# Optimization experiments

Hardware: AMD Instinct MI355X
Metric: run time of the kernel (lower is better)

The kernel has to match this reference:

```python
import jax, jax.numpy as jnp
import numpy as np

FLOW_NUM = 16


def _mlp(z0, p):
    # z0: [B,1]; p = (W1,b1,W2,b2,W3,b3,W4,b4)
    W1, b1, W2, b2, W3, b3, W4, b4 = p
    h = jax.nn.relu(z0 @ W1 + b1)      # [B,10]
    h = jax.nn.relu(h @ W2 + b2)       # [B,10]
    h = jnp.tanh(h @ W3 + b3)          # [B,20]
    return h @ W4 + b4                 # [B,2]


def _forward(inputs, W1, b1, W2, b2, W3, b3, W4, b4):
    x = inputs.astype(jnp.float32)
    z0 = x[:, 0:1]
    z1 = x[:, 1:2]

    def step(carry, p):
        z0_old, z1_old, logdet = carry
        out = _mlp(z0_old, p)                    # [B,2]
        log_scale = out[:, 0:1]                  # log of affine scale
        shift = out[:, 1:2]
        z1_new = jnp.exp(log_scale) * z1_old + shift
        # swap roles for next flow (as in the torch code)
        return (z1_new, z0_old, logdet + log_scale), None

    (z0f, z1f, logdet), _ = jax.lax.scan(
        step, (z0, z1, jnp.zeros_like(z0)), (W1, b1, W2, b2, W3, b3, W4, b4))
    # after the loop: z0_new = z0_old (carry[1]), z1_new = carry[0]
    z0_new, z1_new = z1f, z0f
    # log of standard-normal density product (same math as log(pz))
    log_pz = -0.5 * (z0_new ** 2 + z1_new ** 2) - jnp.log(2.0 * jnp.pi)
    return log_pz + logdet, jnp.concatenate((z0_new, z1_new), axis=1)


def setup_inputs() -> dict:
    key = jax.random.key(0)
    ks = jax.random.split(key, 9)
    B, F = 2097152, FLOW_NUM

    def glorot(k, shape):
        fan_in, fan_out = shape[-2], shape[-1]
        lim = np.sqrt(6.0 / (fan_in + fan_out))
        return jax.random.uniform(k, shape, jnp.float32, -lim, lim)

    return {
        "inputs": jax.random.normal(ks[0], (B, 2), jnp.float32),
        "W1": glorot(ks[1], (F, 1, 10)),  "b1": jnp.zeros((F, 10), jnp.float32),
        "W2": glorot(ks[2], (F, 10, 10)), "b2": jnp.zeros((F, 10), jnp.float32),
        "W3": glorot(ks[3], (F, 10, 20)), "b3": jnp.zeros((F, 20), jnp.float32),
        "W4": glorot(ks[4], (F, 20, 2)),  "b4": jnp.zeros((F, 2), jnp.float32),
    }


def reference(inputs, W1, b1, W2, b2, W3, b3, W4, b4):
    return _forward(inputs, W1, b1, W2, b2, W3, b3, W4, b4)
```

## Files before the change

### kernel.cpp

```cpp
#include <hip/hip_runtime.h>
#include <hip/hip_fp16.h>

#define FLOWS 16
#define NE 2048
#define TAB_DWORDS (FLOWS * NE)
#define TAB_BYTES  (TAB_DWORDS * 4)

__device__ __forceinline__ float2 eval_mlp(int l, float z0,
        const float* __restrict__ W1, const float* __restrict__ B1,
        const float* __restrict__ W2, const float* __restrict__ B2,
        const float* __restrict__ W3, const float* __restrict__ B3,
        const float* __restrict__ W4, const float* __restrict__ B4) {
    const float* w1 = W1 + l * 10;
    const float* c1 = B1 + l * 10;
    const float* w2 = W2 + l * 100;
    const float* c2 = B2 + l * 10;
    const float* w3 = W3 + l * 200;
    const float* c3 = B3 + l * 20;
    const float* w4 = W4 + l * 40;
    const float* c4 = B4 + l * 2;

    float h1[10];
#pragma unroll
    for (int j = 0; j < 10; ++j)
        h1[j] = fmaxf(fmaf(z0, w1[j], c1[j]), 0.0f);

    float h2[10];
#pragma unroll
    for (int j = 0; j < 10; ++j) {
        float acc = c2[j];
#pragma unroll
        for (int i = 0; i < 10; ++i) acc = fmaf(h1[i], w2[i * 10 + j], acc);
        h2[j] = fmaxf(acc, 0.0f);
    }

    float h3[20];
#pragma unroll
    for (int j = 0; j < 20; ++j) {
        float acc = c3[j];
#pragma unroll
        for (int i = 0; i < 10; ++i) acc = fmaf(h2[i], w3[i * 20 + j], acc);
        h3[j] = tanhf(acc);
    }

    float ls = c4[0], sh = c4[1];
#pragma unroll
    for (int i = 0; i < 20; ++i) {
        ls = fmaf(h3[i], w4[i * 2 + 0], ls);
        sh = fmaf(h3[i], w4[i * 2 + 1], sh);
    }
    return make_float2(ls * 1.4426950408889634f, sh);
}

__device__ __forceinline__ float node_z0(int i) {
    float u = fmaf((float)i, 30.0f / 2048.0f, -15.0f);
    float m = 0.125f * (exp2f(fabsf(u)) - 1.0f);
    return u < 0.0f ? -m : m;
}

__global__ __launch_bounds__(256) void build_table_f16(
        const float* __restrict__ W1, const float* __restrict__ B1,
        const float* __restrict__ W2, const float* __restrict__ B2,
        const float* __restrict__ W3, const float* __restrict__ B3,
        const float* __restrict__ W4, const float* __restrict__ B4,
        unsigned int* __restrict__ gtab) {
    int t = blockIdx.x * blockDim.x + threadIdx.x;
    if (t >= TAB_DWORDS) return;
    int l = t >> 11, i = t & (NE - 1);
    float2 r = eval_mlp(l, node_z0(i), W1, B1, W2, B2, W3, B3, W4, B4);
    unsigned int lo = (unsigned int)__half_as_ushort(__float2half_rn(r.x));
    unsigned int hi = (unsigned int)__half_as_ushort(__float2half_rn(r.y));
    gtab[t] = lo | (hi << 16);
}

#define TROWS 8

__global__ __launch_bounds__(1024) void realnvp_lds(
        const float* __restrict__ x,
        const unsigned int* __restrict__ gtab,
        float* __restrict__ out, int nrows) {
    __shared__ unsigned int st[TAB_DWORDS];

    {
        uint4* d = (uint4*)st;
        const uint4* s = (const uint4*)gtab;
        for (int k = threadIdx.x; k < TAB_DWORDS / 4; k += 1024) d[k] = s[k];
    }
    __syncthreads();

    const int rbase = blockIdx.x * (TROWS * 1024) + threadIdx.x;

    float z0[TROWS], z1[TROWS], ld2[TROWS];
#pragma unroll
    for (int r = 0; r < TROWS; ++r) {
        const int row = rbase + r * 1024;
        float2 xv = (row < nrows) ? reinterpret_cast<const float2*>(x)[row]
                                  : make_float2(0.0f, 0.0f);
        z0[r] = xv.x; z1[r] = xv.y; ld2[r] = 0.0f;
    }

    const float INV_DU = 2048.0f / 30.0f;

#pragma unroll 1
    for (int l = 0; l < FLOWS; ++l) {
        const unsigned int* tf = st + (l << 11);

        int   idx[TROWS];
        float fr[TROWS];
#pragma unroll
        for (int r = 0; r < TROWS; ++r) {
            float a  = fmaf(fabsf(z0[r]), 8.0f, 1.0f);
            float lg = __log2f(a);
            float u  = copysignf(lg, z0[r]);
            float fi = fmaf(u, INV_DU, 1024.0f);
            fi = fminf(fmaxf(fi, 0.0f), 2046.99f);
            float t = truncf(fi);
            idx[r]  = (int)t;
            fr[r]   = fi - t;
        }

        unsigned int n0[TROWS], n1[TROWS];
#pragma unroll
        for (int r = 0; r < TROWS; ++r) {
            n0[r] = tf[idx[r]];
            n1[r] = tf[idx[r] + 1];
        }

#pragma unroll
        for (int r = 0; r < TROWS; ++r) {
            float ls0 = __half2float(__ushort_as_half((unsigned short)(n0[r] & 0xffffu)));
            float sh0 = __half2float(__ushort_as_half((unsigned short)(n0[r] >> 16)));
            float ls1 = __half2float(__ushort_as_half((unsigned short)(n1[r] & 0xffffu)));
            float sh1 = __half2float(__ushort_as_half((unsigned short)(n1[r] >> 16)));
            float ls2 = fmaf(fr[r], ls1 - ls0, ls0);
            float sh  = fmaf(fr[r], sh1 - sh0, sh0);
            float t   = fmaf(exp2f(ls2), z1[r], sh);
            z1[r] = z0[r];
            z0[r] = t;
            ld2[r] += ls2;
        }
    }

    float* out_lp = out;
    float2* out_z = reinterpret_cast<float2*>(out + nrows);
#pragma unroll
    for (int r = 0; r < TROWS; ++r) {
        const int row = rbase + r * 1024;
        if (row < nrows) {
            const float z0n = z1[r], z1n = z0[r];
            const float ld  = ld2[r] * 0.6931471805599453f;
            const float lp  = fmaf(-0.5f, fmaf(z0n, z0n, z1n * z1n), -1.8378770664093453f) + ld;
            out_lp[row] = lp;
            out_z[row]  = make_float2(z0n, z1n);
        }
    }
}

#define NE_TAB 2048
#define TAB4_BYTES (FLOWS * NE_TAB * 16)

__global__ __launch_bounds__(256) void build_table(
        const float* __restrict__ W1, const float* __restrict__ B1,
        const float* __restrict__ W2, const float* __restrict__ B2,
        const float* __restrict__ W3, const float* __restrict__ B3,
        const float* __restrict__ W4, const float* __restrict__ B4,
        float4* __restrict__ tab) {
    int t = blockIdx.x * blockDim.x + threadIdx.x;
    if (t >= FLOWS * NE_TAB) return;
    int l = t / NE_TAB, i = t % NE_TAB;
    float2 r0 = eval_mlp(l, node_z0(i),     W1, B1, W2, B2, W3, B3, W4, B4);
    float2 r1 = eval_mlp(l, node_z0(i + 1), W1, B1, W2, B2, W3, B3, W4, B4);
    tab[t] = make_float4(r0.x, r0.y, r1.x, r1.y);
}

__global__ __launch_bounds__(256) void realnvp_tab(
        const float* __restrict__ x,
        const float4* __restrict__ tab,
        float* __restrict__ out, int nrows) {
    const int tid  = blockIdx.x * blockDim.x + threadIdx.x;
    const int base = tid * 4;
    if (base + 4 > nrows) return;

    float z0[4], z1[4], ld2[4];
#pragma unroll
    for (int r = 0; r < 4; ++r) {
        float2 xv = reinterpret_cast<const float2*>(x)[base + r];
        z0[r] = xv.x; z1[r] = xv.y; ld2[r] = 0.0f;
    }
    const float INV_DU = 2048.0f / 30.0f;
#pragma unroll 1
    for (int l = 0; l < FLOWS; ++l) {
        const float4* tf = tab + l * NE_TAB;
        float fr[4]; float4 e[4]; int idx[4];
#pragma unroll
        for (int r = 0; r < 4; ++r) {
            float a  = fmaf(fabsf(z0[r]), 8.0f, 1.0f);
            float lg = __log2f(a);
            float u  = copysignf(lg, z0[r]);
            float fi = fmaf(u, INV_DU, 1024.0f);
            fi = fminf(fmaxf(fi, 0.0f), 2047.999f);
            idx[r] = (int)fi;
            fr[r]  = fi - (float)idx[r];
        }
#pragma unroll
        for (int r = 0; r < 4; ++r) e[r] = tf[idx[r]];
#pragma unroll
        for (int r = 0; r < 4; ++r) {
            float ls2 = fmaf(fr[r], e[r].z - e[r].x, e[r].x);
            float sh  = fmaf(fr[r], e[r].w - e[r].y, e[r].y);
            float t   = fmaf(exp2f(ls2), z1[r], sh);
            z1[r] = z0[r]; z0[r] = t; ld2[r] += ls2;
        }
    }
    float* out_lp = out;
    float2* out_z = reinterpret_cast<float2*>(out + nrows);
#pragma unroll
    for (int r = 0; r < 4; ++r) {
        const float z0n = z1[r], z1n = z0[r];
        const float ld  = ld2[r] * 0.6931471805599453f;
        const float lp  = fmaf(-0.5f, fmaf(z0n, z0n, z1n * z1n), -1.8378770664093453f) + ld;
        out_lp[base + r] = lp;
        out_z[base + r]  = make_float2(z0n, z1n);
    }
}

extern "C" void kernel_launch(void* const* d_in, const int* in_sizes, int n_in,
                              void* d_out, int out_size, void* d_ws, size_t ws_size,
                              hipStream_t stream) {
    const float* x  = (const float*)d_in[0];
    const float* W1 = (const float*)d_in[1];
    const float* B1 = (const float*)d_in[2];
    const float* W2 = (const float*)d_in[3];
    const float* B2 = (const float*)d_in[4];
    const float* W3 = (const float*)d_in[5];
    const float* B3 = (const float*)d_in[6];
    const float* W4 = (const float*)d_in[7];
    const float* B4 = (const float*)d_in[8];
    const int nrows = in_sizes[0] / 2;

    if (ws_size >= (size_t)TAB_BYTES) {
        unsigned int* gtab = (unsigned int*)d_ws;
        build_table_f16<<<(TAB_DWORDS + 255) / 256, 256, 0, stream>>>(
            W1, B1, W2, B2, W3, B3, W4, B4, gtab);
        const int rows_per_block = TROWS * 1024;
        const int blocks = (nrows + rows_per_block - 1) / rows_per_block;
        realnvp_lds<<<blocks, 1024, 0, stream>>>(x, gtab, (float*)d_out, nrows);
    } else if (ws_size >= (size_t)TAB4_BYTES) {
        float4* tab = (float4*)d_ws;
        build_table<<<(FLOWS * NE_TAB + 255) / 256, 256, 0, stream>>>(
            W1, B1, W2, B2, W3, B3, W4, B4, tab);
        const int total_threads = nrows / 4;
        const int blocks = (total_threads + 255) / 256;
        realnvp_tab<<<blocks, 256, 0, stream>>>(x, tab, (float*)d_out, nrows);
    }
}
```

Before: 42.43 us.

## Split waves between LDS fp16 table and global float4 table lookups

```diff
diff --git a/kernel.cpp b/kernel.cpp
--- a/kernel.cpp
+++ b/kernel.cpp
@@ -3,8 +3,19 @@
 
 #define FLOWS 16
 #define NE 2048
-#define TAB_DWORDS (FLOWS * NE)
-#define TAB_BYTES  (TAB_DWORDS * 4)
+#define TAB16_DWORDS (FLOWS * NE)
+#define TAB16_BYTES  (TAB16_DWORDS * 4)
+#define TAB4_BYTES   (FLOWS * NE * 16)
+#define HYBRID_BYTES (TAB16_BYTES + TAB4_BYTES)
+
+#define NWAVES 16
+#define LDS_WAVES 9
+#define TROWS 8
+
+__device__ __forceinline__ float tanh_fast(float x) {
+    float e = __expf(2.0f * x);
+    return 1.0f - 2.0f * __builtin_amdgcn_rcpf(e + 1.0f);
+}
 
 __device__ __forceinline__ float2 eval_mlp(int l, float z0,
         const float* __restrict__ W1, const float* __restrict__ B1,
@@ -40,7 +51,7 @@
         float acc = c3[j];
 #pragma unroll
         for (int i = 0; i < 10; ++i) acc = fmaf(h2[i], w3[i * 20 + j], acc);
-        h3[j] = tanhf(acc);
+        h3[j] = tanh_fast(acc);
     }
 
     float ls = c4[0], sh = c4[1];
@@ -56,6 +67,134 @@
     float u = fmaf((float)i, 30.0f / 2048.0f, -15.0f);
     float m = 0.125f * (exp2f(fabsf(u)) - 1.0f);
     return u < 0.0f ? -m : m;
+}
+
+__global__ __launch_bounds__(256) void build_tables(
+        const float* __restrict__ W1, const float* __restrict__ B1,
+        const float* __restrict__ W2, const float* __restrict__ B2,
+        const float* __restrict__ W3, const float* __restrict__ B3,
+        const float* __restrict__ W4, const float* __restrict__ B4,
+        unsigned int* __restrict__ gtab16, float2* __restrict__ tab4_as_f2) {
+    int t = blockIdx.x * blockDim.x + threadIdx.x;
+    if (t >= FLOWS * (NE + 1)) return;
+    int l = t / (NE + 1), i = t % (NE + 1);
+    float2 r = eval_mlp(l, node_z0(i), W1, B1, W2, B2, W3, B3, W4, B4);
+    if (i < NE) {
+        unsigned int lo = (unsigned int)__half_as_ushort(__float2half_rn(r.x));
+        unsigned int hi = (unsigned int)__half_as_ushort(__float2half_rn(r.y));
+        gtab16[l * NE + i] = lo | (hi << 16);
+        tab4_as_f2[2 * (l * NE + i) + 0] = r;
+    }
+    if (i > 0)
+        tab4_as_f2[2 * (l * NE + i - 1) + 1] = r;
+}
+
+__global__ __launch_bounds__(1024) void realnvp_hybrid(
+        const float* __restrict__ x,
+        const unsigned int* __restrict__ gtab16,
+        const float4* __restrict__ tab4,
+        float* __restrict__ out, int nrows) {
+    __shared__ unsigned int st[TAB16_DWORDS];
+
+    {
+        uint4* d = (uint4*)st;
+        const uint4* s = (const uint4*)gtab16;
+        for (int k = threadIdx.x; k < TAB16_DWORDS / 4; k += 1024) d[k] = s[k];
+    }
+    __syncthreads();
+
+    const int wave = threadIdx.x >> 6;
+    const int lane = threadIdx.x & 63;
+    const int gw   = blockIdx.x * NWAVES + wave;
+    const int rbase = gw * (TROWS * 64) + lane;
+
+    float z0[TROWS], z1[TROWS], ld2[TROWS];
+#pragma unroll
+    for (int r = 0; r < TROWS; ++r) {
+        const int row = rbase + r * 64;
+        float2 xv = (row < nrows) ? reinterpret_cast<const float2*>(x)[row]
+                                  : make_float2(0.0f, 0.0f);
+        z0[r] = xv.x; z1[r] = xv.y; ld2[r] = 0.0f;
+    }
+
+    const float INV_DU = 2048.0f / 30.0f;
+
+    if (wave < LDS_WAVES) {
+#pragma unroll 1
+        for (int l = 0; l < FLOWS; ++l) {
+            const unsigned int* tf = st + (l << 11);
+            int idx[TROWS]; float fr[TROWS];
+#pragma unroll
+            for (int r = 0; r < TROWS; ++r) {
+                float a  = fmaf(fabsf(z0[r]), 8.0f, 1.0f);
+                float lg = __log2f(a);
+                float u  = copysignf(lg, z0[r]);
+                float fi = fmaf(u, INV_DU, 1024.0f);
+                fi = fminf(fmaxf(fi, 0.0f), 2046.99f);
+                float t = truncf(fi);
+                idx[r] = (int)t;
+                fr[r]  = fi - t;
+            }
+            unsigned int n0[TROWS], n1[TROWS];
+#pragma unroll
+            for (int r = 0; r < TROWS; ++r) {
+                n0[r] = tf[idx[r]];
+                n1[r] = tf[idx[r] + 1];
+            }
+#pragma unroll
+            for (int r = 0; r < TROWS; ++r) {
+                float ls0 = __half2float(__ushort_as_half((unsigned short)(n0[r] & 0xffffu)));
+                float sh0 = __half2float(__ushort_as_half((unsigned short)(n0[r] >> 16)));
+                float ls1 = __half2float(__ushort_as_half((unsigned short)(n1[r] & 0xffffu)));
+                float sh1 = __half2float(__ushort_as_half((unsigned short)(n1[r] >> 16)));
+                float ls2 = fmaf(fr[r], ls1 - ls0, ls0);
+                float sh  = fmaf(fr[r], sh1 - sh0, sh0);
+                float t   = fmaf(exp2f(ls2), z1[r], sh);
+                z1[r] = z0[r]; z0[r] = t; ld2[r] += ls2;
+            }
+        }
+    } else {
+#pragma unroll 1
+        for (int l = 0; l < FLOWS; ++l) {
+            const float4* tf = tab4 + (l << 11);
+            int idx[TROWS]; float fr[TROWS];
+#pragma unroll
+            for (int r = 0; r < TROWS; ++r) {
+                float a  = fmaf(fabsf(z0[r]), 8.0f, 1.0f);
+                float lg = __log2f(a);
+                float u  = copysignf(lg, z0[r]);
+                float fi = fmaf(u, INV_DU, 1024.0f);
+                fi = fminf(fmaxf(fi, 0.0f), 2047.999f);
+                float t = truncf(fi);
+                idx[r] = (int)t;
+                fr[r]  = fi - t;
+            }
+            float4 e[TROWS];
+#pragma unroll
+            for (int r = 0; r < TROWS; ++r) e[r] = tf[idx[r]];
+#pragma unroll
+            for (int r = 0; r < TROWS; ++r) {
+                float ls2 = fmaf(fr[r], e[r].z - e[r].x, e[r].x);
+                float sh  = fmaf(fr[r], e[r].w - e[r].y, e[r].y);
+                float t   = fmaf(exp2f(ls2), z1[r], sh);
+                z1[r] = z0[r]; z0[r] = t; ld2[r] += ls2;
+            }
+        }
+    }
+
+    float* out_lp = out;
+    float2* out_z = reinterpret_cast<float2*>(out + nrows);
+#pragma unroll
+    for (int r = 0; r < TROWS; ++r) {
+        const int row = rbase + r * 64;
+        if (row < nrows) {
+            const float z0n = z1[r], z1n = z0[r];
+            const float ld  = ld2[r] * 0.6931471805599453f;
+            const float lp  = fmaf(-0.5f, fmaf(z0n, z0n, z1n * z1n), -1.8378770664093453f) + ld;
+            out_lp[row] = lp;
+            out_z[row]  = make_float2(z0n, z1n);
+        }
+    }
 }
 
 __global__ __launch_bounds__(256) void build_table_f16(
@@ -65,7 +204,7 @@
         const float* __restrict__ W4, const float* __restrict__ B4,
         unsigned int* __restrict__ gtab) {
     int t = blockIdx.x * blockDim.x + threadIdx.x;
-    if (t >= TAB_DWORDS) return;
+    if (t >= TAB16_DWORDS) return;
     int l = t >> 11, i = t & (NE - 1);
     float2 r = eval_mlp(l, node_z0(i), W1, B1, W2, B2, W3, B3, W4, B4);
     unsigned int lo = (unsigned int)__half_as_ushort(__float2half_rn(r.x));
@@ -73,23 +212,19 @@
     gtab[t] = lo | (hi << 16);
 }
 
-#define TROWS 8
-
 __global__ __launch_bounds__(1024) void realnvp_lds(
         const float* __restrict__ x,
         const unsigned int* __restrict__ gtab,
         float* __restrict__ out, int nrows) {
-    __shared__ unsigned int st[TAB_DWORDS];
-
+    __shared__ unsigned int st[TAB16_DWORDS];
     {
         uint4* d = (uint4*)st;
         const uint4* s = (const uint4*)gtab;
-        for (int k = threadIdx.x; k < TAB_DWORDS / 4; k += 1024) d[k] = s[k];
+        for (int k = threadIdx.x; k < TAB16_DWORDS / 4; k += 1024) d[k] = s[k];
     }
     __syncthreads();
 
     const int rbase = blockIdx.x * (TROWS * 1024) + threadIdx.x;
-
     float z0[TROWS], z1[TROWS], ld2[TROWS];
 #pragma unroll
     for (int r = 0; r < TROWS; ++r) {
@@ -98,15 +233,11 @@
                                   : make_float2(0.0f, 0.0f);
         z0[r] = xv.x; z1[r] = xv.y; ld2[r] = 0.0f;
     }
-
     const float INV_DU = 2048.0f / 30.0f;
-
 #pragma unroll 1
     for (int l = 0; l < FLOWS; ++l) {
         const unsigned int* tf = st + (l << 11);
-
-        int   idx[TROWS];
-        float fr[TROWS];
+        int idx[TROWS]; float fr[TROWS];
 #pragma unroll
         for (int r = 0; r < TROWS; ++r) {
             float a  = fmaf(fabsf(z0[r]), 8.0f, 1.0f);
@@ -115,17 +246,11 @@
             float fi = fmaf(u, INV_DU, 1024.0f);
             fi = fminf(fmaxf(fi, 0.0f), 2046.99f);
             float t = truncf(fi);
-            idx[r]  = (int)t;
-            fr[r]   = fi - t;
-        }
-
+            idx[r] = (int)t; fr[r] = fi - t;
+        }
         unsigned int n0[TROWS], n1[TROWS];
 #pragma unroll
-        for (int r = 0; r < TROWS; ++r) {
-            n0[r] = tf[idx[r]];
-            n1[r] = tf[idx[r] + 1];
-        }
-
+        for (int r = 0; r < TROWS; ++r) { n0[r] = tf[idx[r]]; n1[r] = tf[idx[r] + 1]; }
 #pragma unroll
         for (int r = 0; r < TROWS; ++r) {
             float ls0 = __half2float(__ushort_as_half((unsigned short)(n0[r] & 0xffffu)));
@@ -135,12 +260,9 @@
             float ls2 = fmaf(fr[r], ls1 - ls0, ls0);
             float sh  = fmaf(fr[r], sh1 - sh0, sh0);
             float t   = fmaf(exp2f(ls2), z1[r], sh);
-            z1[r] = z0[r];
-            z0[r] = t;
-            ld2[r] += ls2;
-        }
-    }
-
+            z1[r] = z0[r]; z0[r] = t; ld2[r] += ls2;
+        }
+    }
     float* out_lp = out;
     float2* out_z = reinterpret_cast<float2*>(out + nrows);
 #pragma unroll
@@ -153,74 +275,6 @@
             out_lp[row] = lp;
             out_z[row]  = make_float2(z0n, z1n);
         }
-    }
-}
-
-#define NE_TAB 2048
-#define TAB4_BYTES (FLOWS * NE_TAB * 16)
-
-__global__ __launch_bounds__(256) void build_table(
-        const float* __restrict__ W1, const float* __restrict__ B1,
-        const float* __restrict__ W2, const float* __restrict__ B2,
-        const float* __restrict__ W3, const float* __restrict__ B3,
-        const float* __restrict__ W4, const float* __restrict__ B4,
-        float4* __restrict__ tab) {
-    int t = blockIdx.x * blockDim.x + threadIdx.x;
-    if (t >= FLOWS * NE_TAB) return;
-    int l = t / NE_TAB, i = t % NE_TAB;
-    float2 r0 = eval_mlp(l, node_z0(i),     W1, B1, W2, B2, W3, B3, W4, B4);
-    float2 r1 = eval_mlp(l, node_z0(i + 1), W1, B1, W2, B2, W3, B3, W4, B4);
-    tab[t] = make_float4(r0.x, r0.y, r1.x, r1.y);
-}
-
-__global__ __launch_bounds__(256) void realnvp_tab(
-        const float* __restrict__ x,
-        const float4* __restrict__ tab,
-        float* __restrict__ out, int nrows) {
-    const int tid  = blockIdx.x * blockDim.x + threadIdx.x;
-    const int base = tid * 4;
-    if (base + 4 > nrows) return;
-
-    float z0[4], z1[4], ld2[4];
-#pragma unroll
-    for (int r = 0; r < 4; ++r) {
-        float2 xv = reinterpret_cast<const float2*>(x)[base + r];
-        z0[r] = xv.x; z1[r] = xv.y; ld2[r] = 0.0f;
-    }
-    const float INV_DU = 2048.0f / 30.0f;
-#pragma unroll 1
-    for (int l = 0; l < FLOWS; ++l) {
-        const float4* tf = tab + l * NE_TAB;
-        float fr[4]; float4 e[4]; int idx[4];
-#pragma unroll
-        for (int r = 0; r < 4; ++r) {
-            float a  = fmaf(fabsf(z0[r]), 8.0f, 1.0f);
-            float lg = __log2f(a);
-            float u  = copysignf(lg, z0[r]);
-            float fi = fmaf(u, INV_DU, 1024.0f);
-            fi = fminf(fmaxf(fi, 0.0f), 2047.999f);
-            idx[r] = (int)fi;
-            fr[r]  = fi - (float)idx[r];
-        }
-#pragma unroll
-        for (int r = 0; r < 4; ++r) e[r] = tf[idx[r]];
-#pragma unroll
-        for (int r = 0; r < 4; ++r) {
-            float ls2 = fmaf(fr[r], e[r].z - e[r].x, e[r].x);
-            float sh  = fmaf(fr[r], e[r].w - e[r].y, e[r].y);
-            float t   = fmaf(exp2f(ls2), z1[r], sh);
-            z1[r] = z0[r]; z0[r] = t; ld2[r] += ls2;
-        }
-    }
-    float* out_lp = out;
-    float2* out_z = reinterpret_cast<float2*>(out + nrows);
-#pragma unroll
-    for (int r = 0; r < 4; ++r) {
-        const float z0n = z1[r], z1n = z0[r];
-        const float ld  = ld2[r] * 0.6931471805599453f;
-        const float lp  = fmaf(-0.5f, fmaf(z0n, z0n, z1n * z1n), -1.8378770664093453f) + ld;
-        out_lp[base + r] = lp;
-        out_z[base + r]  = make_float2(z0n, z1n);
     }
 }
 
@@ -238,19 +292,21 @@
     const float* B4 = (const float*)d_in[8];
     const int nrows = in_sizes[0] / 2;
 
-    if (ws_size >= (size_t)TAB_BYTES) {
+    if (ws_size >= (size_t)HYBRID_BYTES) {
+        unsigned int* gtab16 = (unsigned int*)d_ws;
+        float4* tab4 = (float4*)((char*)d_ws + TAB16_BYTES);
+        const int nb = (FLOWS * (NE + 1) + 255) / 256;
+        build_tables<<<nb, 256, 0, stream>>>(W1, B1, W2, B2, W3, B3, W4, B4,
+                                             gtab16, (float2*)tab4);
+        const int rows_per_block = NWAVES * TROWS * 64;
+        const int blocks = (nrows + rows_per_block - 1) / rows_per_block;
+        realnvp_hybrid<<<blocks, 1024, 0, stream>>>(x, gtab16, tab4, (float*)d_out, nrows);
+    } else if (ws_size >= (size_t)TAB16_BYTES) {
         unsigned int* gtab = (unsigned int*)d_ws;
-        build_table_f16<<<(TAB_DWORDS + 255) / 256, 256, 0, stream>>>(
+        build_table_f16<<<(TAB16_DWORDS + 255) / 256, 256, 0, stream>>>(
             W1, B1, W2, B2, W3, B3, W4, B4, gtab);
         const int rows_per_block = TROWS * 1024;
         const int blocks = (nrows + rows_per_block - 1) / rows_per_block;
         realnvp_lds<<<blocks, 1024, 0, stream>>>(x, gtab, (float*)d_out, nrows);
-    } else if (ws_size >= (size_t)TAB4_BYTES) {
-        float4* tab = (float4*)d_ws;
-        build_table<<<(FLOWS * NE_TAB + 255) / 256, 256, 0, stream>>>(
-            W1, B1, W2, B2, W3, B3, W4, B4, tab);
-        const int total_threads = nrows / 4;
-        const int blocks = (total_threads + 255) / 256;
-        realnvp_tab<<<blocks, 256, 0, stream>>>(x, tab, (float*)d_out, nrows);
-    }
-}
+    }
+}
```

After: 44.65 us. 5.2% more time.
